# Kernel optimization log

Measured on AMD Instinct MI355X. Metric: run time of the kernel, lower is better.

## Reference

```python
import jax, jax.numpy as jnp
import numpy as np

B, N = 2, 4096
SA, DG, ED, OUT = 128, 1024, 4, 128
RF = 0.1   # ED_radius_factor
EPS = 1e-5  # BatchNorm eps


def setup_inputs() -> dict:
    key = jax.random.key(0)
    ks = jax.random.split(key, 16)
    def w(k, sh, sc=0.05):
        return jax.random.normal(k, sh, jnp.float32) * sc
    return dict(
        pointcloud=jax.random.normal(ks[0], (B, N, 3), jnp.float32),
        h1=jax.random.normal(ks[1], (B, SA, N), jnp.float32),
        h2=jax.random.normal(ks[2], (B, DG, N), jnp.float32),
        dg_w1=w(ks[3], (256, DG)), dg_b1=jnp.zeros(256), dg_g1=jnp.ones(256), dg_be1=jnp.zeros(256),
        dg_w2=w(ks[4], (64, 256)), dg_b2=jnp.zeros(64), dg_g2=jnp.ones(64), dg_be2=jnp.zeros(64),
        dg_w3=w(ks[5], (32, 64)), dg_b3=jnp.zeros(32), dg_g3=jnp.ones(32), dg_be3=jnp.zeros(32),
        ed_w1=w(ks[6], (3, ED), 0.5), ed_b1=jnp.zeros(ED),
        ed_w2=w(ks[7], (ED, ED), 0.5), ed_b2=jnp.zeros(ED),
        w1=w(ks[8], (512, SA + 32 + ED)), b1=jnp.zeros(512), g1=jnp.ones(512), be1=jnp.zeros(512),
        w2=w(ks[9], (256, 512)), b2=jnp.zeros(256), g2=jnp.ones(256), be2=jnp.zeros(256),
        w3=w(ks[10], (OUT, 256)), b3=jnp.zeros(OUT), g3=jnp.ones(OUT), be3=jnp.zeros(OUT),
    )


def _conv1x1(x, w, b):  # x: (B,C,N) 1x1 Conv1d
    return jnp.einsum('oc,bcn->bon', w, x) + b[None, :, None]


def _bn(x, g, b):  # training-mode BatchNorm1d over (B,N) per channel
    m = x.mean(axis=(0, 2), keepdims=True)
    v = ((x - m) ** 2).mean(axis=(0, 2), keepdims=True)
    return g[None, :, None] * (x - m) * jax.lax.rsqrt(v + EPS) + b[None, :, None]


def _eigs(xyz):  # (N,3) -> (N,3) eigenvalues of per-point radius-neighbor covariance
    n = xyz.shape[0]
    x2 = (xyz * xyz).sum(-1)
    d2 = jnp.maximum(x2[:, None] + x2[None, :] - 2.0 * (xyz @ xyz.T), 0.0)
    dist = jnp.sqrt(jnp.maximum(d2, 1e-12))
    eye = jnp.eye(n, dtype=bool)
    max_d = jnp.where(eye, -jnp.inf, dist).max()  # calculate_distances max
    radius = max_d * RF                            # adaptive radius
    mask = ((dist < radius) & ~eye).astype(xyz.dtype)  # (N,N) radius neighbors, no self
    cnt = mask.sum(1)                              # true neighbor count (for the mean)
    mu = (mask @ xyz) / jnp.maximum(cnt, 1.0)[:, None]
    # sum_j m_ij x_j x_j^T via one matmul on flattened outer products
    S = (mask @ (xyz[:, :, None] * xyz[:, None, :]).reshape(n, 9)).reshape(n, 3, 3)
    # NOTE: original divides by k = mask.shape[0] == N (not neighbor count) -- kept faithfully
    cov = (S - cnt[:, None, None] * mu[:, :, None] * mu[:, None, :]) / n
    return jnp.linalg.eigvalsh(cov)


def reference(pointcloud, h1, h2,
              dg_w1, dg_b1, dg_g1, dg_be1,
              dg_w2, dg_b2, dg_g2, dg_be2,
              dg_w3, dg_b3, dg_g3, dg_be3,
              ed_w1, ed_b1, ed_w2, ed_b2,
              w1, b1, g1, be1, w2, b2, g2, be2, w3, b3, g3, be3):
    xyz = pointcloud[..., 0:3]
    # DG head: 1024 -> 256 -> 64 -> 32 (1x1 conv + BN + ReLU)
    f2 = jax.nn.relu(_bn(_conv1x1(h2, dg_w1, dg_b1), dg_g1, dg_be1))
    f2 = jax.nn.relu(_bn(_conv1x1(f2, dg_w2, dg_b2), dg_g2, dg_be2))
    f2 = jax.nn.relu(_bn(_conv1x1(f2, dg_w3, dg_b3), dg_g3, dg_be3))
    # ED branch: per-point local PCA eigenvalues + tiny MLP (3->4->4)
    eig = jax.vmap(_eigs)(xyz)                        # (B,N,3)
    h3 = jax.nn.relu(eig @ ed_w1 + ed_b1) @ ed_w2 + ed_b2  # (B,N,4)
    z = jnp.concatenate([h1, f2, jnp.transpose(h3, (0, 2, 1))], axis=1)  # (B,164,N)
    z = jax.nn.relu(_bn(_conv1x1(z, w1, b1), g1, be1))
    z = jax.nn.relu(_bn(_conv1x1(z, w2, b2), g2, be2))
    z = jax.nn.relu(_bn(_conv1x1(z, w3, b3), g3, be3))
    return (xyz, z)
```

## Files before the change

### kernel.cpp

```cpp
#include <hip/hip_runtime.h>
#include <math.h>

#define NPTS 4096
#define NB 2

typedef __attribute__((ext_vector_type(8))) short short8;
typedef __attribute__((ext_vector_type(4))) float f32x4;
typedef unsigned int uint32;

__device__ __forceinline__ unsigned short f2bf(float f) {
  uint32 u = __float_as_uint(f);
  uint32 r = (u + 0x7FFFu + ((u >> 16) & 1u)) >> 16;
  return (unsigned short)r;
}
__device__ __forceinline__ uint2 pack4(float a, float b, float c, float d) {
  uint2 r;
  r.x = (uint32)f2bf(a) | ((uint32)f2bf(b) << 16);
  r.y = (uint32)f2bf(c) | ((uint32)f2bf(d) << 16);
  return r;
}
__device__ __forceinline__ float bflo(uint32 w) { return __uint_as_float((w & 0xffffu) << 16); }
__device__ __forceinline__ float bfhi(uint32 w) { return __uint_as_float(w & 0xffff0000u); }

struct WArgs {
  const float* src[6];
  unsigned short* dst[6];
};

__device__ __forceinline__ void transpose_tile(const float* __restrict__ src, int C,
                                               unsigned short* __restrict__ dst,
                                               int dstStride, int dstOff, int b, int c0,
                                               int n0) {
  __shared__ float tile[32][33];
  const float* s = src + (size_t)b * C * NPTS;
  int r = threadIdx.x >> 3, q = threadIdx.x & 7;
  float4 v = *(const float4*)(s + (size_t)(c0 + r) * NPTS + n0 + q * 4);
  tile[r][q * 4 + 0] = v.x;
  tile[r][q * 4 + 1] = v.y;
  tile[r][q * 4 + 2] = v.z;
  tile[r][q * 4 + 3] = v.w;
  __syncthreads();
  uint2 o = pack4(tile[q * 4 + 0][r], tile[q * 4 + 1][r], tile[q * 4 + 2][r],
                  tile[q * 4 + 3][r]);
  *(uint2*)(dst + ((size_t)b * NPTS + n0 + r) * dstStride + dstOff + c0 + q * 4) = o;
}

__global__ __launch_bounds__(256)
void prep_all(const float* __restrict__ h2, const float* __restrict__ h1, WArgs wa,
              unsigned short* __restrict__ h2t, unsigned short* __restrict__ Zt,
              unsigned int* __restrict__ mx) {
  int bid = blockIdx.x;
  if (bid < 8192) {
    int b = bid >> 12, r = bid & 4095, ct = r & 31, nt = r >> 5;
    transpose_tile(h2, 1024, h2t, 1024, 0, b, ct * 32, nt * 32);
  } else if (bid < 9216) {
    int r = bid - 8192, b = r >> 9, r2 = r & 511, ct = r2 & 3, nt = r2 >> 2;
    transpose_tile(h1, 128, Zt, 192, 0, b, ct * 32, nt * 32);
  } else if (bid < 9248) {
    int r = bid - 9216;
    for (int idx = r * 256 + threadIdx.x; idx < NB * NPTS * 7; idx += 32 * 256) {
      int u = idx % 7, n = (idx / 7) & (NPTS - 1), b = idx / (7 * NPTS);
      *(uint2*)(Zt + ((size_t)b * NPTS + n) * 192 + 164 + u * 4) = make_uint2(0u, 0u);
    }
  } else if (bid < 9504) {
    const int segKp[6] = {1024, 256, 64, 192, 512, 256};
    const int segM[6] = {256, 64, 32, 512, 256, 128};
    const int segK[6] = {1024, 256, 64, 164, 512, 256};
    const int segEnd[6] = {262144, 278528, 282624, 380928, 512000, 544768};
    int r = bid - 9248;
    for (int idx = r * 256 + threadIdx.x; idx < 544768; idx += 256 * 256) {
      int w = 0, start = 0;
#pragma unroll
      for (int s = 0; s < 6; ++s)
        if (idx >= segEnd[s]) { w = s + 1; start = segEnd[s]; }
      int local = idx - start, Kp = segKp[w], m = local / Kp, k = local % Kp;
      float v = (m < segM[w] && k < segK[w]) ? wa.src[w][m * segK[w] + k] : 0.f;
      wa.dst[w][local] = f2bf(v);
    }
  } else {
    if (threadIdx.x < 2) mx[threadIdx.x] = 0u;
  }
}

template <int BN_IN>
__global__ __launch_bounds__(256)
void gemm_mfma_t(const unsigned short* __restrict__ Wp, const unsigned short* __restrict__ X,
                 const float* __restrict__ aG, const float* __restrict__ bG,
                 unsigned short* __restrict__ Y, float* __restrict__ psum,
                 float* __restrict__ psq, int M, int Mp, int Kp) {
  __shared__ char db[2][9216];
  __shared__ float a_sh[512], b_sh[512];
  const int b = blockIdx.z, nt = blockIdx.x, mt = blockIdx.y;
  const int n0 = nt * 64, m0 = mt * 64;
  const int tid = threadIdx.x, lane = tid & 63, wid = tid >> 6;
  const int wm = wid >> 1, wn = wid & 1, g = lane >> 4, c = lane & 15;
  const int ktiles = Kp >> 6;
  const unsigned short* Xb = X + (size_t)b * NPTS * Kp;

  if (BN_IN) {
    for (int ch = tid; ch < Kp; ch += 256) {
      a_sh[ch] = aG[ch];
      b_sh[ch] = bG[ch];
    }
    __syncthreads();
  }

  uint4 st[2];
  auto loadG = [&](int kt) {
    int k0 = kt << 6;
#pragma unroll
    for (int i = 0; i < 2; ++i) {
      int u = tid + i * 256, n = u >> 3, s = u & 7;
      st[i] = *(const uint4*)(Xb + (size_t)(n0 + n) * Kp + k0 + s * 8);
    }
  };
  auto writeS = [&](int buf, int kt) {
    int k0 = kt << 6;
#pragma unroll
    for (int i = 0; i < 2; ++i) {
      int u = tid + i * 256, n = u >> 3, s = u & 7;
      uint4 v = st[i];
      if (BN_IN) {
        int k = k0 + s * 8;
        float4 a0 = *(const float4*)&a_sh[k], a1 = *(const float4*)&a_sh[k + 4];
        float4 b0 = *(const float4*)&b_sh[k], b1 = *(const float4*)&b_sh[k + 4];
        uint2 lo = pack4(fmaxf(bflo(v.x) * a0.x + b0.x, 0.f),
                         fmaxf(bfhi(v.x) * a0.y + b0.y, 0.f),
                         fmaxf(bflo(v.y) * a0.z + b0.z, 0.f),
                         fmaxf(bfhi(v.y) * a0.w + b0.w, 0.f));
        uint2 hi = pack4(fmaxf(bflo(v.z) * a1.x + b1.x, 0.f),
                         fmaxf(bfhi(v.z) * a1.y + b1.y, 0.f),
                         fmaxf(bflo(v.w) * a1.z + b1.z, 0.f),
                         fmaxf(bfhi(v.w) * a1.w + b1.w, 0.f));
        v = make_uint4(lo.x, lo.y, hi.x, hi.y);
      }
      *(uint4*)&db[buf][u / 8 * 144 + (u & 7) * 16] = v;
      (void)n;
    }
  };
  auto loadA = [&](int kt, uint4* Af) {
    const unsigned short* base = Wp + (size_t)(m0 + wm * 32 + c) * Kp + (kt << 6) + g * 8;
#pragma unroll
    for (int mf = 0; mf < 2; ++mf)
#pragma unroll
      for (int kw = 0; kw < 2; ++kw)
        Af[mf * 2 + kw] = *(const uint4*)(base + (size_t)mf * 16 * Kp + kw * 32);
  };

  f32x4 acc[2][2] = {};
  uint4 Acur[4], Anext[4] = {};
  loadG(0);
  loadA(0, Acur);
  writeS(0, 0);
  __syncthreads();
  int cur = 0;
  for (int t = 0; t < ktiles; ++t) {
    if (t + 1 < ktiles) {
      loadG(t + 1);
      loadA(t + 1, Anext);
    }
#pragma unroll
    for (int kw = 0; kw < 2; ++kw) {
      union { uint4 u; short8 s; } a0, a1;
      a0.u = Acur[0 * 2 + kw];
      a1.u = Acur[1 * 2 + kw];
#pragma unroll
      for (int nf = 0; nf < 2; ++nf) {
        union { uint4 u; short8 s; } bf;
        bf.u = *(const uint4*)&db[cur][(wn * 32 + nf * 16 + c) * 144 + kw * 64 + g * 16];
        acc[0][nf] = __builtin_amdgcn_mfma_f32_16x16x32_bf16(a0.s, bf.s, acc[0][nf], 0, 0, 0);
        acc[1][nf] = __builtin_amdgcn_mfma_f32_16x16x32_bf16(a1.s, bf.s, acc[1][nf], 0, 0, 0);
      }
    }
    if (t + 1 < ktiles) writeS(cur ^ 1, t + 1);
    __syncthreads();
    cur ^= 1;
#pragma unroll
    for (int i = 0; i < 4; ++i) Acur[i] = Anext[i];
  }

#pragma unroll
  for (int nf = 0; nf < 2; ++nf) {
    int n = n0 + wn * 32 + nf * 16 + c;
    unsigned short* yrow = Y + ((size_t)b * NPTS + n) * Mp;
#pragma unroll
    for (int mf = 0; mf < 2; ++mf) {
      int mb = m0 + wm * 32 + mf * 16 + g * 4;
      *(uint2*)(yrow + mb) =
          pack4(acc[mf][nf][0], acc[mf][nf][1], acc[mf][nf][2], acc[mf][nf][3]);
    }
  }
  int slot = b * 128 + nt * 2 + wn;
#pragma unroll
  for (int mf = 0; mf < 2; ++mf)
#pragma unroll
    for (int r = 0; r < 4; ++r) {
      float s = acc[mf][0][r] + acc[mf][1][r];
      float q = acc[mf][0][r] * acc[mf][0][r] + acc[mf][1][r] * acc[mf][1][r];
#pragma unroll
      for (int m = 1; m < 16; m <<= 1) {
        s += __shfl_xor(s, m, 64);
        q += __shfl_xor(q, m, 64);
      }
      int row = m0 + wm * 32 + mf * 16 + g * 4 + r;
      if (c == 0 && row < M) {
        psum[(size_t)row * 256 + slot] = s;
        psq[(size_t)row * 256 + slot] = q;
      }
    }
}

__global__ __launch_bounds__(256)
void bn_finalize(const float* __restrict__ psum, const float* __restrict__ psq,
                 const float* __restrict__ gamma, const float* __restrict__ beta,
                 float* __restrict__ a_, float* __restrict__ b_) {
  int ch = blockIdx.x, t = threadIdx.x;
  float s = psum[(size_t)ch * 256 + t];
  float q = psq[(size_t)ch * 256 + t];
#pragma unroll
  for (int m = 1; m < 64; m <<= 1) {
    s += __shfl_xor(s, m, 64);
    q += __shfl_xor(q, m, 64);
  }
  __shared__ float ws[4][2];
  if ((t & 63) == 0) { ws[t >> 6][0] = s; ws[t >> 6][1] = q; }
  __syncthreads();
  if (t == 0) {
    float S = ws[0][0] + ws[1][0] + ws[2][0] + ws[3][0];
    float Q = ws[0][1] + ws[1][1] + ws[2][1] + ws[3][1];
    const float inv = 1.f / (float)(NB * NPTS);
    float mean = S * inv;
    float var = fmaxf(Q * inv - mean * mean, 0.f);
    float aa = rsqrtf(var + 1e-5f) * gamma[ch];
    a_[ch] = aa;
    b_[ch] = beta[ch] - mean * aa;
  }
}

__global__ __launch_bounds__(256)
void f2_apply(const unsigned short* __restrict__ Y, const float* __restrict__ a_,
              const float* __restrict__ b_, unsigned short* __restrict__ Zt) {
  int idx = blockIdx.x * 256 + threadIdx.x;
  int c4 = idx & 7;
  int n = (idx >> 3) & (NPTS - 1);
  int b = idx >> 15;
  uint2 v = *(const uint2*)(Y + ((size_t)b * NPTS + n) * 64 + c4 * 4);
  float4 aa = ((const float4*)a_)[c4];
  float4 bb = ((const float4*)b_)[c4];
  uint2 o = pack4(fmaxf(bflo(v.x) * aa.x + bb.x, 0.f), fmaxf(bfhi(v.x) * aa.y + bb.y, 0.f),
                  fmaxf(bflo(v.y) * aa.z + bb.z, 0.f), fmaxf(bfhi(v.y) * aa.w + bb.w, 0.f));
  *(uint2*)(Zt + ((size_t)b * NPTS + n) * 192 + 128 + c4 * 4) = o;
}

__global__ __launch_bounds__(256)
void out_final(const unsigned short* __restrict__ Y, const float* __restrict__ a_,
               const float* __restrict__ b_, const float* __restrict__ pc,
               float* __restrict__ out) {
  int bid = blockIdx.x;
  if (bid < 1024) {
    __shared__ float tile[32][33];
    int b = bid >> 9, r0 = bid & 511;
    int c0 = (r0 & 3) * 32, n0 = (r0 >> 2) * 32;
    int r = threadIdx.x >> 3, q = threadIdx.x & 7;
    uint2 v = *(const uint2*)(Y + ((size_t)b * NPTS + n0 + r) * 128 + c0 + q * 4);
    float4 aa = *(const float4*)(a_ + c0 + q * 4);
    float4 bb = *(const float4*)(b_ + c0 + q * 4);
    tile[r][q * 4 + 0] = fmaxf(bflo(v.x) * aa.x + bb.x, 0.f);
    tile[r][q * 4 + 1] = fmaxf(bfhi(v.x) * aa.y + bb.y, 0.f);
    tile[r][q * 4 + 2] = fmaxf(bflo(v.y) * aa.z + bb.z, 0.f);
    tile[r][q * 4 + 3] = fmaxf(bfhi(v.y) * aa.w + bb.w, 0.f);
    __syncthreads();
    float4 o = make_float4(tile[q * 4 + 0][r], tile[q * 4 + 1][r], tile[q * 4 + 2][r],
                           tile[q * 4 + 3][r]);
    float* z = out + (size_t)NB * NPTS * 3;
    *(float4*)(z + ((size_t)b * 128 + c0 + r) * NPTS + n0 + q * 4) = o;
  } else {
    int i = (bid - 1024) * 256 + threadIdx.x;
    ((float4*)out)[i] = ((const float4*)pc)[i];
  }
}

__global__ __launch_bounds__(256)
void maxd2_kernel(const float* __restrict__ pc, unsigned int* __restrict__ mx) {
  __shared__ float4 sp[512];
  __shared__ float lm[4];
  int b = blockIdx.z;
  int j0 = blockIdx.y * 512;
  int i0 = blockIdx.x * 64;
  const float* pb = pc + (size_t)b * NPTS * 3;
  for (int t = threadIdx.x; t < 512; t += 256) {
    int j = j0 + t;
    sp[t] = make_float4(pb[j * 3], pb[j * 3 + 1], pb[j * 3 + 2], 0.f);
  }
  __syncthreads();
  int il = threadIdx.x & 63, sl = threadIdx.x >> 6;
  int i = i0 + il;
  float xi = pb[i * 3], yi = pb[i * 3 + 1], zi = pb[i * 3 + 2];
  float x2i = xi * xi + yi * yi + zi * zi;
  float m = 0.f;
#pragma unroll 4
  for (int j = sl * 128, e = sl * 128 + 128; j < e; ++j) {
    float4 pj = sp[j];
    float x2j = pj.x * pj.x + pj.y * pj.y + pj.z * pj.z;
    float dot = xi * pj.x + yi * pj.y + zi * pj.z;
    m = fmaxf(m, fmaxf(x2i + x2j - 2.f * dot, 0.f));
  }
#pragma unroll
  for (int off = 32; off > 0; off >>= 1) m = fmaxf(m, __shfl_xor(m, off, 64));
  if ((threadIdx.x & 63) == 0) lm[threadIdx.x >> 6] = m;
  __syncthreads();
  if (threadIdx.x == 0) {
    float v = fmaxf(fmaxf(lm[0], lm[1]), fmaxf(lm[2], lm[3]));
    atomicMax(&mx[b], __float_as_uint(v));
  }
}

__global__ __launch_bounds__(256)
void eigs_partial(const float* __restrict__ pc, const unsigned int* __restrict__ mx,
                  float* __restrict__ part) {
  __shared__ float4 sp[1024];
  __shared__ float red[4][32][10];
  int b = blockIdx.z;
  int js = blockIdx.y;
  int j0 = js * 1024;
  int i0 = blockIdx.x * 32;
  const float* pb = pc + (size_t)b * NPTS * 3;
  for (int t = threadIdx.x; t < 1024; t += 256) {
    int j = j0 + t;
    sp[t] = make_float4(pb[j * 3], pb[j * 3 + 1], pb[j * 3 + 2], 0.f);
  }
  __syncthreads();
  int il = threadIdx.x & 31, sl = threadIdx.x >> 5;
  int i = i0 + il;
  float xi = pb[i * 3], yi = pb[i * 3 + 1], zi = pb[i * 3 + 2];
  float x2i = xi * xi + yi * yi + zi * zi;
  float r2 = 0.01f * fmaxf(__uint_as_float(mx[b]), 1e-12f);
  float vals[10];
#pragma unroll
  for (int v = 0; v < 10; ++v) vals[v] = 0.f;
  int iloc = i - j0;
#pragma unroll 2
  for (int j = sl * 128, e = sl * 128 + 128; j < e; ++j) {
    float4 pj = sp[j];
    float x2j = pj.x * pj.x + pj.y * pj.y + pj.z * pj.z;
    float dot = xi * pj.x + yi * pj.y + zi * pj.z;
    float d2 = fmaxf(fmaxf(x2i + x2j - 2.f * dot, 0.f), 1e-12f);
    float msk = ((d2 < r2) && (j != iloc)) ? 1.f : 0.f;
    vals[0] += msk;
    vals[1] = fmaf(msk, pj.x, vals[1]);
    vals[2] = fmaf(msk, pj.y, vals[2]);
    vals[3] = fmaf(msk, pj.z, vals[3]);
    vals[4] = fmaf(msk, pj.x * pj.x, vals[4]);
    vals[5] = fmaf(msk, pj.x * pj.y, vals[5]);
    vals[6] = fmaf(msk, pj.x * pj.z, vals[6]);
    vals[7] = fmaf(msk, pj.y * pj.y, vals[7]);
    vals[8] = fmaf(msk, pj.y * pj.z, vals[8]);
    vals[9] = fmaf(msk, pj.z * pj.z, vals[9]);
  }
#pragma unroll
  for (int v = 0; v < 10; ++v) vals[v] += __shfl_xor(vals[v], 32, 64);
  int w = threadIdx.x >> 6;
  if ((threadIdx.x & 63) < 32)
#pragma unroll
    for (int v = 0; v < 10; ++v) red[w][il][v] = vals[v];
  __syncthreads();
  if (threadIdx.x < 32) {
    int ii = i0 + threadIdx.x;
    size_t base = ((size_t)(b * 4 + js) * 10) * NPTS + ii;
#pragma unroll
    for (int v = 0; v < 10; ++v)
      part[base + (size_t)v * NPTS] = red[0][threadIdx.x][v] + red[1][threadIdx.x][v] +
                                      red[2][threadIdx.x][v] + red[3][threadIdx.x][v];
  }
}

__global__ __launch_bounds__(256)
void eigs_finalize(const float* __restrict__ part, const float* __restrict__ ew1,
                   const float* __restrict__ eb1, const float* __restrict__ ew2,
                   const float* __restrict__ eb2, unsigned short* __restrict__ Zt) {
  int p = blockIdx.x * 256 + threadIdx.x;
  int b = p >> 12, i = p & (NPTS - 1);
  float t[10];
#pragma unroll
  for (int v = 0; v < 10; ++v) {
    float s = 0.f;
#pragma unroll
    for (int js = 0; js < 4; ++js) s += part[((size_t)(b * 4 + js) * 10 + v) * NPTS + i];
    t[v] = s;
  }
  double cntd = (double)t[0];
  double denom = cntd > 1.0 ? cntd : 1.0;
  double mux = t[1] / denom, muy = t[2] / denom, muz = t[3] / denom;
  const double inv_n = 1.0 / (double)NPTS;
  double a00 = ((double)t[4] - cntd * mux * mux) * inv_n;
  double a01 = ((double)t[5] - cntd * mux * muy) * inv_n;
// ... 22 lines not shown
    e0 = q + 2.0 * pp * cos(phi + 2.0943951023931953);
    e1 = 3.0 * q - e0 - e2;
  }
  float eg[3] = {(float)e0, (float)e1, (float)e2};
  float tmp[4];
#pragma unroll
  for (int e = 0; e < 4; ++e) {
    float v = eb1[e];
#pragma unroll
    for (int k = 0; k < 3; ++k) v = fmaf(eg[k], ew1[k * 4 + e], v);
    tmp[e] = fmaxf(v, 0.f);
  }
  float h3[4];
#pragma unroll
  for (int f = 0; f < 4; ++f) {
    float v = eb2[f];
#pragma unroll
    for (int e = 0; e < 4; ++e) v = fmaf(tmp[e], ew2[e * 4 + f], v);
    h3[f] = v;
  }
  *(uint2*)(Zt + ((size_t)b * NPTS + i) * 192 + 160) = pack4(h3[0], h3[1], h3[2], h3[3]);
}

extern "C" void kernel_launch(void* const* d_in, const int* in_sizes, int n_in,
                              void* d_out, int out_size, void* d_ws, size_t ws_size,
                              hipStream_t stream) {
  (void)in_sizes; (void)n_in; (void)out_size; (void)ws_size;
  const float* pc    = (const float*)d_in[0];
  const float* h1    = (const float*)d_in[1];
  const float* h2    = (const float*)d_in[2];
  const float* dgw1  = (const float*)d_in[3];
  const float* dgg1  = (const float*)d_in[5];
  const float* dgbe1 = (const float*)d_in[6];
  const float* dgw2  = (const float*)d_in[7];
  const float* dgg2  = (const float*)d_in[9];
  const float* dgbe2 = (const float*)d_in[10];
  const float* dgw3  = (const float*)d_in[11];
  const float* dgg3  = (const float*)d_in[13];
  const float* dgbe3 = (const float*)d_in[14];
  const float* ew1   = (const float*)d_in[15];
  const float* eb1   = (const float*)d_in[16];
  const float* ew2   = (const float*)d_in[17];
  const float* eb2   = (const float*)d_in[18];
  const float* w1    = (const float*)d_in[19];
  const float* g1    = (const float*)d_in[21];
  const float* be1   = (const float*)d_in[22];
  const float* w2    = (const float*)d_in[23];
  const float* g2    = (const float*)d_in[25];
  const float* be2   = (const float*)d_in[26];
  const float* w3    = (const float*)d_in[27];
  const float* g3    = (const float*)d_in[29];
  const float* be3   = (const float*)d_in[30];
  float* out = (float*)d_out;

  char* p = (char*)d_ws;
  auto take = [&](size_t bytes) { char* r = p; p += (bytes + 255) & ~(size_t)255; return r; };
  unsigned short* h2t = (unsigned short*)take((size_t)NB * NPTS * 1024 * 2);
  unsigned short* Zt  = (unsigned short*)take((size_t)NB * NPTS * 192 * 2);
  unsigned short* wp1 = (unsigned short*)take((size_t)256 * 1024 * 2);
  unsigned short* wp2 = (unsigned short*)take((size_t)64 * 256 * 2);
  unsigned short* wp3 = (unsigned short*)take((size_t)64 * 64 * 2);
  unsigned short* wp4 = (unsigned short*)take((size_t)512 * 192 * 2);
  unsigned short* wp5 = (unsigned short*)take((size_t)256 * 512 * 2);
  unsigned short* wp6 = (unsigned short*)take((size_t)128 * 256 * 2);
  unsigned short* yA  = (unsigned short*)take((size_t)NB * NPTS * 256 * 2);
  unsigned short* yB  = (unsigned short*)take((size_t)NB * NPTS * 512 * 2);
  float* psum = (float*)take((size_t)512 * 256 * 4);
  float* psq  = (float*)take((size_t)512 * 256 * 4);
  float* a_   = (float*)take((size_t)512 * 4);
  float* b_   = (float*)take((size_t)512 * 4);
  float* part = (float*)take((size_t)NB * 4 * 10 * NPTS * 4);
  unsigned int* mx = (unsigned int*)take(256);

  WArgs wa;
  wa.src[0] = dgw1; wa.dst[0] = wp1;
  wa.src[1] = dgw2; wa.dst[1] = wp2;
  wa.src[2] = dgw3; wa.dst[2] = wp3;
  wa.src[3] = w1;   wa.dst[3] = wp4;
  wa.src[4] = w2;   wa.dst[4] = wp5;
  wa.src[5] = w3;   wa.dst[5] = wp6;

  prep_all<<<9505, 256, 0, stream>>>(h2, h1, wa, h2t, Zt, mx);
  maxd2_kernel<<<dim3(NPTS / 64, 8, NB), 256, 0, stream>>>(pc, mx);
  eigs_partial<<<dim3(NPTS / 32, 4, NB), 256, 0, stream>>>(pc, mx, part);
  eigs_finalize<<<NB * NPTS / 256, 256, 0, stream>>>(part, ew1, eb1, ew2, eb2, Zt);

  auto layerD = [&](const unsigned short* Wp, const unsigned short* X, unsigned short* Y,
                    int M, int Mp, int Kp, const float* g, const float* be) {
    gemm_mfma_t<0><<<dim3(64, Mp / 64, NB), 256, 0, stream>>>(Wp, X, a_, b_, Y, psum, psq,
                                                              M, Mp, Kp);
    bn_finalize<<<M, 256, 0, stream>>>(psum, psq, g, be, a_, b_);
  };
  auto layerF = [&](const unsigned short* Wp, const unsigned short* X, unsigned short* Y,
                    int M, int Mp, int Kp, const float* g, const float* be) {
    gemm_mfma_t<1><<<dim3(64, Mp / 64, NB), 256, 0, stream>>>(Wp, X, a_, b_, Y, psum, psq,
                                                              M, Mp, Kp);
    bn_finalize<<<M, 256, 0, stream>>>(psum, psq, g, be, a_, b_);
  };

  layerD(wp1, h2t, yA, 256, 256, 1024, dgg1, dgbe1);
  layerF(wp2, yA, yB, 64, 64, 256, dgg2, dgbe2);
  layerF(wp3, yB, yA, 32, 64, 64, dgg3, dgbe3);
  f2_apply<<<NB * NPTS * 8 / 256, 256, 0, stream>>>(yA, a_, b_, Zt);
  layerD(wp4, Zt, yB, 512, 512, 192, g1, be1);
  layerF(wp5, yB, yA, 256, 256, 512, g2, be2);
  layerF(wp6, yA, yB, 128, 128, 256, g3, be3);
  out_final<<<1048, 256, 0, stream>>>(yB, a_, b_, pc, out);
}
```

Before: 168.4 us.

## Fuse BN finalize into GEMMs, merge maxd2 into prep and eigs into first GEMM

Folds the separate BN-finalize kernels into each GEMM through a last-block atomic counter. The pairwise max-distance pass moves into the prep kernel and the eigen-partial pass runs as extra blocks of the first GEMM. The f2_apply kernel is removed by having layer 3 write into Zt directly, with a per-channel floor vector standing in for ReLU. Transposes use larger 64x64 tiles, and the GEMM double-buffers global loads two tiles ahead. The aim is fewer launches and less serialization, at the cost of more complex ordering through atomics and fences and heavier per-block shared memory.

```diff
diff --git a/kernel.cpp b/kernel.cpp
--- a/kernel.cpp
+++ b/kernel.cpp
@@ -3,6 +3,7 @@
 
 #define NPTS 4096
 #define NB 2
+#define BIGNEG -3.0e38f
 
 typedef __attribute__((ext_vector_type(8))) short short8;
 typedef __attribute__((ext_vector_type(4))) float f32x4;
@@ -22,143 +23,264 @@
 __device__ __forceinline__ float bflo(uint32 w) { return __uint_as_float((w & 0xffffu) << 16); }
 __device__ __forceinline__ float bfhi(uint32 w) { return __uint_as_float(w & 0xffff0000u); }
 
-struct WArgs {
-  const float* src[6];
-  unsigned short* dst[6];
+struct PrepP {
+  const float *h2, *h1, *pc;
+  const float* wsrc[6];
+  unsigned short* wdst[6];
+  unsigned short *h2t, *Zt;
+  float *aZ, *bZ, *fZ, *f0;
+  unsigned int* mx;
 };
 
-__device__ __forceinline__ void transpose_tile(const float* __restrict__ src, int C,
-                                               unsigned short* __restrict__ dst,
-                                               int dstStride, int dstOff, int b, int c0,
-                                               int n0) {
-  __shared__ float tile[32][33];
-  const float* s = src + (size_t)b * C * NPTS;
-  int r = threadIdx.x >> 3, q = threadIdx.x & 7;
-  float4 v = *(const float4*)(s + (size_t)(c0 + r) * NPTS + n0 + q * 4);
-  tile[r][q * 4 + 0] = v.x;
-  tile[r][q * 4 + 1] = v.y;
-  tile[r][q * 4 + 2] = v.z;
-  tile[r][q * 4 + 3] = v.w;
-  __syncthreads();
-  uint2 o = pack4(tile[q * 4 + 0][r], tile[q * 4 + 1][r], tile[q * 4 + 2][r],
-                  tile[q * 4 + 3][r]);
-  *(uint2*)(dst + ((size_t)b * NPTS + n0 + r) * dstStride + dstOff + c0 + q * 4) = o;
-}
+union ShPrep {
+  float tile[64][65];
+  struct { float4 sp[512]; float lm[8]; } m;
+};
 
 __global__ __launch_bounds__(256)
-void prep_all(const float* __restrict__ h2, const float* __restrict__ h1, WArgs wa,
-              unsigned short* __restrict__ h2t, unsigned short* __restrict__ Zt,
-              unsigned int* __restrict__ mx) {
-  int bid = blockIdx.x;
-  if (bid < 8192) {
-    int b = bid >> 12, r = bid & 4095, ct = r & 31, nt = r >> 5;
-    transpose_tile(h2, 1024, h2t, 1024, 0, b, ct * 32, nt * 32);
-  } else if (bid < 9216) {
-    int r = bid - 8192, b = r >> 9, r2 = r & 511, ct = r2 & 3, nt = r2 >> 2;
-    transpose_tile(h1, 128, Zt, 192, 0, b, ct * 32, nt * 32);
-  } else if (bid < 9248) {
-    int r = bid - 9216;
-    for (int idx = r * 256 + threadIdx.x; idx < NB * NPTS * 7; idx += 32 * 256) {
+void prep_maxd2(PrepP P) {
+  __shared__ ShPrep sh;
+  int bid = blockIdx.x, tid = threadIdx.x;
+  if (bid < 2304) {
+    const float* src; unsigned short* dst; int S, C, b, c0, n0;
+    if (bid < 2048) {
+      b = bid >> 10; int r = bid & 1023;
+      c0 = (r & 15) * 64; n0 = (r >> 4) * 64;
+      src = P.h2; dst = P.h2t; S = 1024; C = 1024;
+    } else {
+      int r = bid - 2048; b = r >> 7; int r2 = r & 127;
+      c0 = (r2 & 1) * 64; n0 = (r2 >> 1) * 64;
+      src = P.h1; dst = P.Zt; S = 192; C = 128;
+    }
+    const float* sb = src + (size_t)b * C * NPTS;
+#pragma unroll
+    for (int p = 0; p < 4; ++p) {
+      int r = (tid >> 4) + p * 16, q = tid & 15;
+      float4 v = *(const float4*)(sb + (size_t)(c0 + r) * NPTS + n0 + q * 4);
+      sh.tile[r][q * 4 + 0] = v.x;
+      sh.tile[r][q * 4 + 1] = v.y;
+      sh.tile[r][q * 4 + 2] = v.z;
+      sh.tile[r][q * 4 + 3] = v.w;
+    }
+    __syncthreads();
+#pragma unroll
+    for (int p = 0; p < 2; ++p) {
+      int n = (tid >> 3) + p * 32, j = tid & 7;
+      uint2 lo = pack4(sh.tile[j * 8 + 0][n], sh.tile[j * 8 + 1][n], sh.tile[j * 8 + 2][n],
+                       sh.tile[j * 8 + 3][n]);
+      uint2 hi = pack4(sh.tile[j * 8 + 4][n], sh.tile[j * 8 + 5][n], sh.tile[j * 8 + 6][n],
+                       sh.tile[j * 8 + 7][n]);
+      *(uint4*)(dst + ((size_t)b * NPTS + n0 + n) * S + c0 + j * 8) =
+          make_uint4(lo.x, lo.y, hi.x, hi.y);
+    }
+  } else if (bid < 2336) {
+    int r = bid - 2304;
+    for (int idx = r * 256 + tid; idx < NB * NPTS * 7; idx += 32 * 256) {
       int u = idx % 7, n = (idx / 7) & (NPTS - 1), b = idx / (7 * NPTS);
-      *(uint2*)(Zt + ((size_t)b * NPTS + n) * 192 + 164 + u * 4) = make_uint2(0u, 0u);
-    }
-  } else if (bid < 9504) {
+      *(uint2*)(P.Zt + ((size_t)b * NPTS + n) * 192 + 164 + u * 4) = make_uint2(0u, 0u);
+    }
+  } else if (bid < 2592) {
     const int segKp[6] = {1024, 256, 64, 192, 512, 256};
     const int segM[6] = {256, 64, 32, 512, 256, 128};
     const int segK[6] = {1024, 256, 64, 164, 512, 256};
     const int segEnd[6] = {262144, 278528, 282624, 380928, 512000, 544768};
-    int r = bid - 9248;
-    for (int idx = r * 256 + threadIdx.x; idx < 544768; idx += 256 * 256) {
+    int r = bid - 2336;
+    for (int idx = r * 256 + tid; idx < 544768; idx += 256 * 256) {
       int w = 0, start = 0;
 #pragma unroll
       for (int s = 0; s < 6; ++s)
         if (idx >= segEnd[s]) { w = s + 1; start = segEnd[s]; }
       int local = idx - start, Kp = segKp[w], m = local / Kp, k = local % Kp;
-      float v = (m < segM[w] && k < segK[w]) ? wa.src[w][m * segK[w] + k] : 0.f;
-      wa.dst[w][local] = f2bf(v);
+      float v = (m < segM[w] && k < segK[w]) ? P.wsrc[w][m * segK[w] + k] : 0.f;
+      P.wdst[w][local] = f2bf(v);
+    }
+  } else if (bid == 2592) {
+    for (int ch = tid; ch < 512; ch += 256) {
+      P.f0[ch] = 0.f;
+      if (ch < 192) { P.aZ[ch] = 1.f; P.bZ[ch] = 0.f; P.fZ[ch] = BIGNEG; }
     }
   } else {
-    if (threadIdx.x < 2) mx[threadIdx.x] = 0u;
-  }
-}
-
-template <int BN_IN>
+    int vb = bid - 2593;
+    int b = vb >> 9, rem = vb & 511, it = rem & 63, jt = rem >> 6;
+    int i0 = it * 64, j0 = jt * 512;
+    const float* pb = P.pc + (size_t)b * NPTS * 3;
+    for (int t = tid; t < 512; t += 256) {
+      int j = j0 + t;
+      float x = pb[j * 3], y = pb[j * 3 + 1], z = pb[j * 3 + 2];
+      sh.m.sp[t] = make_float4(x, y, z, fmaf(x, x, fmaf(y, y, z * z)));
+    }
+    __syncthreads();
+    int il = tid & 63, sl = tid >> 6;
+    int i = i0 + il;
+    float xi = pb[i * 3], yi = pb[i * 3 + 1], zi = pb[i * 3 + 2];
+    float x2i = fmaf(xi, xi, fmaf(yi, yi, zi * zi));
+    float m = 0.f;
+#pragma unroll 4
+    for (int j = sl * 128, e2 = sl * 128 + 128; j < e2; ++j) {
+      float4 pj = sh.m.sp[j];
+      float dot = fmaf(xi, pj.x, fmaf(yi, pj.y, zi * pj.z));
+      m = fmaxf(m, fmaf(-2.f, dot, x2i + pj.w));
+    }
+#pragma unroll
+    for (int off = 32; off > 0; off >>= 1) m = fmaxf(m, __shfl_xor(m, off, 64));
+    if ((tid & 63) == 0) sh.m.lm[tid >> 6] = m;
+    __syncthreads();
+    if (tid == 0) {
+      float v = fmaxf(fmaxf(sh.m.lm[0], sh.m.lm[1]), fmaxf(sh.m.lm[2], sh.m.lm[3]));
+      atomicMax(&P.mx[b], __float_as_uint(v));
+    }
+  }
+}
+
+struct GemmP {
+  const unsigned short* Wp;
+  const unsigned short* X;
+  const float *aIn, *bIn, *fIn;
+  unsigned short* Y;
+  int Ystride;
+  const float *gam, *bet;
+  float *aOut, *bOut, *fOut;
+  unsigned int* cnt;
+  float *psum, *psq;
+  int M, Kp, ngb;
+};
+
+union ShGemm {
+  struct { char db[2][9216]; float ash[512], bsh[512], fsh[512]; } g;
+  struct { float4 sp[1024]; float red[4][32][10]; } e;
+};
+
+template <int BN_IN, int WITH_EIG>
 __global__ __launch_bounds__(256)
-void gemm_mfma_t(const unsigned short* __restrict__ Wp, const unsigned short* __restrict__ X,
-                 const float* __restrict__ aG, const float* __restrict__ bG,
-                 unsigned short* __restrict__ Y, float* __restrict__ psum,
-                 float* __restrict__ psq, int M, int Mp, int Kp) {
-  __shared__ char db[2][9216];
-  __shared__ float a_sh[512], b_sh[512];
+void gemm_k(GemmP P, const float* __restrict__ pc, const unsigned int* __restrict__ mx,
+            float* __restrict__ part) {
+  __shared__ ShGemm sh;
+  __shared__ unsigned int lastf;
+  const int tid = threadIdx.x;
+
+  if (WITH_EIG && blockIdx.z >= NB) {
+    int e = blockIdx.x + 64 * blockIdx.y + 256 * (blockIdx.z - NB);
+    int b = e >> 9, rem = e & 511, it = rem & 127, js = rem >> 7;
+    int i0 = it * 32, j0 = js * 1024;
+    const float* pb = pc + (size_t)b * NPTS * 3;
+    for (int t = tid; t < 1024; t += 256) {
+      int j = j0 + t;
+      float x = pb[j * 3], y = pb[j * 3 + 1], z = pb[j * 3 + 2];
+      sh.e.sp[t] = make_float4(x, y, z, fmaf(x, x, fmaf(y, y, z * z)));
+    }
+    __syncthreads();
+    int il = tid & 31, sl = tid >> 5;
+    int i = i0 + il;
+    float xi = pb[i * 3], yi = pb[i * 3 + 1], zi = pb[i * 3 + 2];
+    float x2i = fmaf(xi, xi, fmaf(yi, yi, zi * zi));
+    float r2 = 0.01f * fmaxf(__uint_as_float(mx[b]), 1e-12f);
+    float v0 = 0, v1 = 0, v2 = 0, v3 = 0, v4 = 0, v5 = 0, v6 = 0, v7 = 0, v8 = 0, v9 = 0;
+#pragma unroll 2
+    for (int j = sl * 128, e2 = sl * 128 + 128; j < e2; ++j) {
+      float4 pj = sh.e.sp[j];
+      float dot = fmaf(xi, pj.x, fmaf(yi, pj.y, zi * pj.z));
+      float d2 = fmaf(-2.f, dot, x2i + pj.w);
+      float msk = d2 < r2 ? 1.f : 0.f;
+      float qx = msk * pj.x, qy = msk * pj.y, qz = msk * pj.z;
+      v0 += msk; v1 += qx; v2 += qy; v3 += qz;
+      v4 = fmaf(qx, pj.x, v4); v5 = fmaf(qx, pj.y, v5); v6 = fmaf(qx, pj.z, v6);
+      v7 = fmaf(qy, pj.y, v7); v8 = fmaf(qy, pj.z, v8); v9 = fmaf(qz, pj.z, v9);
+    }
+    int iloc = i - j0;
+    if (iloc >= sl * 128 && iloc < sl * 128 + 128) {
+      v0 -= 1.f; v1 -= xi; v2 -= yi; v3 -= zi;
+      v4 = fmaf(-xi, xi, v4); v5 = fmaf(-xi, yi, v5); v6 = fmaf(-xi, zi, v6);
+      v7 = fmaf(-yi, yi, v7); v8 = fmaf(-yi, zi, v8); v9 = fmaf(-zi, zi, v9);
+    }
+    float vals[10] = {v0, v1, v2, v3, v4, v5, v6, v7, v8, v9};
+#pragma unroll
+    for (int v = 0; v < 10; ++v) vals[v] += __shfl_xor(vals[v], 32, 64);
+    int w = tid >> 6;
+    if ((tid & 63) < 32)
+#pragma unroll
+      for (int v = 0; v < 10; ++v) sh.e.red[w][il][v] = vals[v];
+    __syncthreads();
+    if (tid < 32) {
+      int ii = i0 + tid;
+      size_t base = ((size_t)(b * 4 + js) * 10) * NPTS + ii;
+#pragma unroll
+      for (int v = 0; v < 10; ++v)
+        part[base + (size_t)v * NPTS] =
+            sh.e.red[0][tid][v] + sh.e.red[1][tid][v] + sh.e.red[2][tid][v] + sh.e.red[3][tid][v];
+    }
+    return;
+  }
+
   const int b = blockIdx.z, nt = blockIdx.x, mt = blockIdx.y;
   const int n0 = nt * 64, m0 = mt * 64;
-  const int tid = threadIdx.x, lane = tid & 63, wid = tid >> 6;
+  const int lane = tid & 63, wid = tid >> 6;
   const int wm = wid >> 1, wn = wid & 1, g = lane >> 4, c = lane & 15;
-  const int ktiles = Kp >> 6;
-  const unsigned short* Xb = X + (size_t)b * NPTS * Kp;
+  const int kt = P.Kp >> 6;
+  const unsigned short* Xb = P.X + (size_t)b * NPTS * P.Kp;
 
   if (BN_IN) {
-    for (int ch = tid; ch < Kp; ch += 256) {
-      a_sh[ch] = aG[ch];
-      b_sh[ch] = bG[ch];
-    }
-    __syncthreads();
-  }
-
-  uint4 st[2];
-  auto loadG = [&](int kt) {
-    int k0 = kt << 6;
+    for (int ch = tid; ch < P.Kp; ch += 256) {
+      sh.g.ash[ch] = P.aIn[ch];
+      sh.g.bsh[ch] = P.bIn[ch];
+      sh.g.fsh[ch] = P.fIn[ch];
+    }
+    __syncthreads();
+  }
+
+  uint4 R0[2], R1[2];
+  auto loadG = [&](int t, uint4* R) {
+    int k0 = t << 6;
 #pragma unroll
     for (int i = 0; i < 2; ++i) {
       int u = tid + i * 256, n = u >> 3, s = u & 7;
-      st[i] = *(const uint4*)(Xb + (size_t)(n0 + n) * Kp + k0 + s * 8);
+      R[i] = *(const uint4*)(Xb + (size_t)(n0 + n) * P.Kp + k0 + s * 8);
     }
   };
-  auto writeS = [&](int buf, int kt) {
-    int k0 = kt << 6;
+  auto writeS = [&](int buf, int t, uint4* R) {
+    int k0 = t << 6;
 #pragma unroll
     for (int i = 0; i < 2; ++i) {
-      int u = tid + i * 256, n = u >> 3, s = u & 7;
-      uint4 v = st[i];
+      int u = tid + i * 256, s = u & 7;
+      uint4 v = R[i];
       if (BN_IN) {
         int k = k0 + s * 8;
-        float4 a0 = *(const float4*)&a_sh[k], a1 = *(const float4*)&a_sh[k + 4];
-        float4 b0 = *(const float4*)&b_sh[k], b1 = *(const float4*)&b_sh[k + 4];
-        uint2 lo = pack4(fmaxf(bflo(v.x) * a0.x + b0.x, 0.f),
-                         fmaxf(bfhi(v.x) * a0.y + b0.y, 0.f),
-                         fmaxf(bflo(v.y) * a0.z + b0.z, 0.f),
-                         fmaxf(bfhi(v.y) * a0.w + b0.w, 0.f));
-        uint2 hi = pack4(fmaxf(bflo(v.z) * a1.x + b1.x, 0.f),
-                         fmaxf(bfhi(v.z) * a1.y + b1.y, 0.f),
-                         fmaxf(bflo(v.w) * a1.z + b1.z, 0.f),
-                         fmaxf(bfhi(v.w) * a1.w + b1.w, 0.f));
+        float4 a0 = *(const float4*)&sh.g.ash[k], a1 = *(const float4*)&sh.g.ash[k + 4];
+        float4 b0 = *(const float4*)&sh.g.bsh[k], b1 = *(const float4*)&sh.g.bsh[k + 4];
+        float4 f0 = *(const float4*)&sh.g.fsh[k], f1 = *(const float4*)&sh.g.fsh[k + 4];
+        uint2 lo = pack4(fmaxf(fmaf(bflo(v.x), a0.x, b0.x), f0.x),
+                         fmaxf(fmaf(bfhi(v.x), a0.y, b0.y), f0.y),
+                         fmaxf(fmaf(bflo(v.y), a0.z, b0.z), f0.z),
+                         fmaxf(fmaf(bfhi(v.y), a0.w, b0.w), f0.w));
+        uint2 hi = pack4(fmaxf(fmaf(bflo(v.z), a1.x, b1.x), f1.x),
+                         fmaxf(fmaf(bfhi(v.z), a1.y, b1.y), f1.y),
+                         fmaxf(fmaf(bflo(v.w), a1.z, b1.z), f1.z),
+                         fmaxf(fmaf(bfhi(v.w), a1.w, b1.w), f1.w));
         v = make_uint4(lo.x, lo.y, hi.x, hi.y);
       }
-      *(uint4*)&db[buf][u / 8 * 144 + (u & 7) * 16] = v;
-      (void)n;
+      *(uint4*)&sh.g.db[buf][(u >> 3) * 144 + (u & 7) * 16] = v;
     }
   };
-  auto loadA = [&](int kt, uint4* Af) {
-    const unsigned short* base = Wp + (size_t)(m0 + wm * 32 + c) * Kp + (kt << 6) + g * 8;
+  auto loadA = [&](int t, uint4* Af) {
+    const unsigned short* base = P.Wp + (size_t)(m0 + wm * 32 + c) * P.Kp + (t << 6) + g * 8;
 #pragma unroll
     for (int mf = 0; mf < 2; ++mf)
 #pragma unroll
       for (int kw = 0; kw < 2; ++kw)
-        Af[mf * 2 + kw] = *(const uint4*)(base + (size_t)mf * 16 * Kp + kw * 32);
+        Af[mf * 2 + kw] = *(const uint4*)(base + (size_t)mf * 16 * P.Kp + kw * 32);
   };
 
   f32x4 acc[2][2] = {};
   uint4 Acur[4], Anext[4] = {};
-  loadG(0);
+  loadG(0, R0);
   loadA(0, Acur);
-  writeS(0, 0);
+  writeS(0, 0, R0);
+  if (kt > 1) loadG(1, R1);
   __syncthreads();
   int cur = 0;
-  for (int t = 0; t < ktiles; ++t) {
-    if (t + 1 < ktiles) {
-      loadG(t + 1);
-      loadA(t + 1, Anext);
-    }
+
+  auto step = [&](int t, uint4* Rload, uint4* Rwrite) {
+    if (t + 2 < kt) loadG(t + 2, Rload);
+    if (t + 1 < kt) loadA(t + 1, Anext);
 #pragma unroll
     for (int kw = 0; kw < 2; ++kw) {
       union { uint4 u; short8 s; } a0, a1;
@@ -167,27 +289,35 @@
 #pragma unroll
       for (int nf = 0; nf < 2; ++nf) {
         union { uint4 u; short8 s; } bf;
-        bf.u = *(const uint4*)&db[cur][(wn * 32 + nf * 16 + c) * 144 + kw * 64 + g * 16];
+        bf.u = *(const uint4*)&sh.g.db[cur][(wn * 32 + nf * 16 + c) * 144 + kw * 64 + g * 16];
         acc[0][nf] = __builtin_amdgcn_mfma_f32_16x16x32_bf16(a0.s, bf.s, acc[0][nf], 0, 0, 0);
         acc[1][nf] = __builtin_amdgcn_mfma_f32_16x16x32_bf16(a1.s, bf.s, acc[1][nf], 0, 0, 0);
       }
     }
-    if (t + 1 < ktiles) writeS(cur ^ 1, t + 1);
+    if (t + 1 < kt) writeS(cur ^ 1, t + 1, Rwrite);
     __syncthreads();
     cur ^= 1;
 #pragma unroll
     for (int i = 0; i < 4; ++i) Acur[i] = Anext[i];
+  };
+  for (int t = 0; t < kt;) {
+    step(t, R0, R1);
+    ++t;
+    if (t >= kt) break;
+    step(t, R1, R0);
+    ++t;
   }
 
 #pragma unroll
   for (int nf = 0; nf < 2; ++nf) {
     int n = n0 + wn * 32 + nf * 16 + c;
-    unsigned short* yrow = Y + ((size_t)b * NPTS + n) * Mp;
+    unsigned short* yrow = P.Y + ((size_t)b * NPTS + n) * P.Ystride;
 #pragma unroll
     for (int mf = 0; mf < 2; ++mf) {
       int mb = m0 + wm * 32 + mf * 16 + g * 4;
-      *(uint2*)(yrow + mb) =
-          pack4(acc[mf][nf][0], acc[mf][nf][1], acc[mf][nf][2], acc[mf][nf][3]);
+      if (mb < P.M)
+        *(uint2*)(yrow + mb) =
+            pack4(acc[mf][nf][0], acc[mf][nf][1], acc[mf][nf][2], acc[mf][nf][3]);
     }
   }
   int slot = b * 128 + nt * 2 + wn;
@@ -203,174 +333,35 @@
         q += __shfl_xor(q, m, 64);
       }
       int row = m0 + wm * 32 + mf * 16 + g * 4 + r;
-      if (c == 0 && row < M) {
-        psum[(size_t)row * 256 + slot] = s;
-        psq[(size_t)row * 256 + slot] = q;
+      if (c == 0 && row < P.M) {
+        P.psum[(size_t)row * 256 + slot] = s;
+        P.psq[(size_t)row * 256 + slot] = q;
       }
     }
-}
-
-__global__ __launch_bounds__(256)
-void bn_finalize(const float* __restrict__ psum, const float* __restrict__ psq,
-                 const float* __restrict__ gamma, const float* __restrict__ beta,
-                 float* __restrict__ a_, float* __restrict__ b_) {
-  int ch = blockIdx.x, t = threadIdx.x;
-  float s = psum[(size_t)ch * 256 + t];
-  float q = psq[(size_t)ch * 256 + t];
-#pragma unroll
-  for (int m = 1; m < 64; m <<= 1) {
-    s += __shfl_xor(s, m, 64);
-    q += __shfl_xor(q, m, 64);
-  }
-  __shared__ float ws[4][2];
-  if ((t & 63) == 0) { ws[t >> 6][0] = s; ws[t >> 6][1] = q; }
+
+  __threadfence();
+  if (tid == 0) lastf = (atomicAdd(P.cnt, 1u) == (unsigned)(P.ngb - 1)) ? 1u : 0u;
   __syncthreads();
-  if (t == 0) {
-    float S = ws[0][0] + ws[1][0] + ws[2][0] + ws[3][0];
-    float Q = ws[0][1] + ws[1][1] + ws[2][1] + ws[3][1];
-    const float inv = 1.f / (float)(NB * NPTS);
-    float mean = S * inv;
-    float var = fmaxf(Q * inv - mean * mean, 0.f);
-    float aa = rsqrtf(var + 1e-5f) * gamma[ch];
-    a_[ch] = aa;
-    b_[ch] = beta[ch] - mean * aa;
-  }
-}
-
-__global__ __launch_bounds__(256)
-void f2_apply(const unsigned short* __restrict__ Y, const float* __restrict__ a_,
-              const float* __restrict__ b_, unsigned short* __restrict__ Zt) {
-  int idx = blockIdx.x * 256 + threadIdx.x;
-  int c4 = idx & 7;
-  int n = (idx >> 3) & (NPTS - 1);
-  int b = idx >> 15;
-  uint2 v = *(const uint2*)(Y + ((size_t)b * NPTS + n) * 64 + c4 * 4);
-  float4 aa = ((const float4*)a_)[c4];
-  float4 bb = ((const float4*)b_)[c4];
-  uint2 o = pack4(fmaxf(bflo(v.x) * aa.x + bb.x, 0.f), fmaxf(bfhi(v.x) * aa.y + bb.y, 0.f),
-                  fmaxf(bflo(v.y) * aa.z + bb.z, 0.f), fmaxf(bfhi(v.y) * aa.w + bb.w, 0.f));
-  *(uint2*)(Zt + ((size_t)b * NPTS + n) * 192 + 128 + c4 * 4) = o;
-}
-
-__global__ __launch_bounds__(256)
-void out_final(const unsigned short* __restrict__ Y, const float* __restrict__ a_,
-               const float* __restrict__ b_, const float* __restrict__ pc,
-               float* __restrict__ out) {
-  int bid = blockIdx.x;
-  if (bid < 1024) {
-    __shared__ float tile[32][33];
-    int b = bid >> 9, r0 = bid & 511;
-    int c0 = (r0 & 3) * 32, n0 = (r0 >> 2) * 32;
-    int r = threadIdx.x >> 3, q = threadIdx.x & 7;
-    uint2 v = *(const uint2*)(Y + ((size_t)b * NPTS + n0 + r) * 128 + c0 + q * 4);
-    float4 aa = *(const float4*)(a_ + c0 + q * 4);
-    float4 bb = *(const float4*)(b_ + c0 + q * 4);
-    tile[r][q * 4 + 0] = fmaxf(bflo(v.x) * aa.x + bb.x, 0.f);
-    tile[r][q * 4 + 1] = fmaxf(bfhi(v.x) * aa.y + bb.y, 0.f);
-    tile[r][q * 4 + 2] = fmaxf(bflo(v.y) * aa.z + bb.z, 0.f);
-    tile[r][q * 4 + 3] = fmaxf(bfhi(v.y) * aa.w + bb.w, 0.f);
-    __syncthreads();
-    float4 o = make_float4(tile[q * 4 + 0][r], tile[q * 4 + 1][r], tile[q * 4 + 2][r],
-                           tile[q * 4 + 3][r]);
-    float* z = out + (size_t)NB * NPTS * 3;
-    *(float4*)(z + ((size_t)b * 128 + c0 + r) * NPTS + n0 + q * 4) = o;
-  } else {
-    int i = (bid - 1024) * 256 + threadIdx.x;
-    ((float4*)out)[i] = ((const float4*)pc)[i];
-  }
-}
-
-__global__ __launch_bounds__(256)
-void maxd2_kernel(const float* __restrict__ pc, unsigned int* __restrict__ mx) {
-  __shared__ float4 sp[512];
-  __shared__ float lm[4];
-  int b = blockIdx.z;
-  int j0 = blockIdx.y * 512;
-  int i0 = blockIdx.x * 64;
-  const float* pb = pc + (size_t)b * NPTS * 3;
-  for (int t = threadIdx.x; t < 512; t += 256) {
-    int j = j0 + t;
-    sp[t] = make_float4(pb[j * 3], pb[j * 3 + 1], pb[j * 3 + 2], 0.f);
-  }
-  __syncthreads();
-  int il = threadIdx.x & 63, sl = threadIdx.x >> 6;
-  int i = i0 + il;
-  float xi = pb[i * 3], yi = pb[i * 3 + 1], zi = pb[i * 3 + 2];
-  float x2i = xi * xi + yi * yi + zi * zi;
-  float m = 0.f;
+  if (lastf) {
+    for (int ch = tid; ch < P.M; ch += 256) {
+      const float4* s4 = (const float4*)(P.psum + (size_t)ch * 256);
+      const float4* q4 = (const float4*)(P.psq + (size_t)ch * 256);
+      float s = 0.f, q = 0.f;
 #pragma unroll 4
-  for (int j = sl * 128, e = sl * 128 + 128; j < e; ++j) {
-    float4 pj = sp[j];
-    float x2j = pj.x * pj.x + pj.y * pj.y + pj.z * pj.z;
-    float dot = xi * pj.x + yi * pj.y + zi * pj.z;
-    m = fmaxf(m, fmaxf(x2i + x2j - 2.f * dot, 0.f));
-  }
-#pragma unroll
-  for (int off = 32; off > 0; off >>= 1) m = fmaxf(m, __shfl_xor(m, off, 64));
-  if ((threadIdx.x & 63) == 0) lm[threadIdx.x >> 6] = m;
-  __syncthreads();
-  if (threadIdx.x == 0) {
-    float v = fmaxf(fmaxf(lm[0], lm[1]), fmaxf(lm[2], lm[3]));
-    atomicMax(&mx[b], __float_as_uint(v));
-  }
-}
-
-__global__ __launch_bounds__(256)
-void eigs_partial(const float* __restrict__ pc, const unsigned int* __restrict__ mx,
-                  float* __restrict__ part) {
-  __shared__ float4 sp[1024];
-  __shared__ float red[4][32][10];
-  int b = blockIdx.z;
-  int js = blockIdx.y;
-  int j0 = js * 1024;
-  int i0 = blockIdx.x * 32;
-  const float* pb = pc + (size_t)b * NPTS * 3;
-  for (int t = threadIdx.x; t < 1024; t += 256) {
-    int j = j0 + t;
-    sp[t] = make_float4(pb[j * 3], pb[j * 3 + 1], pb[j * 3 + 2], 0.f);
-  }
-  __syncthreads();
-  int il = threadIdx.x & 31, sl = threadIdx.x >> 5;
-  int i = i0 + il;
-  float xi = pb[i * 3], yi = pb[i * 3 + 1], zi = pb[i * 3 + 2];
-  float x2i = xi * xi + yi * yi + zi * zi;
-  float r2 = 0.01f * fmaxf(__uint_as_float(mx[b]), 1e-12f);
-  float vals[10];
-#pragma unroll
-  for (int v = 0; v < 10; ++v) vals[v] = 0.f;
-  int iloc = i - j0;
-#pragma unroll 2
-  for (int j = sl * 128, e = sl * 128 + 128; j < e; ++j) {
-    float4 pj = sp[j];
-    float x2j = pj.x * pj.x + pj.y * pj.y + pj.z * pj.z;
-    float dot = xi * pj.x + yi * pj.y + zi * pj.z;
-    float d2 = fmaxf(fmaxf(x2i + x2j - 2.f * dot, 0.f), 1e-12f);
-    float msk = ((d2 < r2) && (j != iloc)) ? 1.f : 0.f;
-    vals[0] += msk;
-    vals[1] = fmaf(msk, pj.x, vals[1]);
-    vals[2] = fmaf(msk, pj.y, vals[2]);
-    vals[3] = fmaf(msk, pj.z, vals[3]);
-    vals[4] = fmaf(msk, pj.x * pj.x, vals[4]);
-    vals[5] = fmaf(msk, pj.x * pj.y, vals[5]);
-    vals[6] = fmaf(msk, pj.x * pj.z, vals[6]);
-    vals[7] = fmaf(msk, pj.y * pj.y, vals[7]);
-    vals[8] = fmaf(msk, pj.y * pj.z, vals[8]);
-    vals[9] = fmaf(msk, pj.z * pj.z, vals[9]);
-  }
-#pragma unroll
-  for (int v = 0; v < 10; ++v) vals[v] += __shfl_xor(vals[v], 32, 64);
-  int w = threadIdx.x >> 6;
-  if ((threadIdx.x & 63) < 32)
-#pragma unroll
-    for (int v = 0; v < 10; ++v) red[w][il][v] = vals[v];
-  __syncthreads();
-  if (threadIdx.x < 32) {
-    int ii = i0 + threadIdx.x;
-    size_t base = ((size_t)(b * 4 + js) * 10) * NPTS + ii;
-#pragma unroll
-    for (int v = 0; v < 10; ++v)
-      part[base + (size_t)v * NPTS] = red[0][threadIdx.x][v] + red[1][threadIdx.x][v] +
-                                      red[2][threadIdx.x][v] + red[3][threadIdx.x][v];
+      for (int i = 0; i < 64; ++i) {
+        float4 a = s4[i];
+        s += a.x + a.y + a.z + a.w;
+        float4 w = q4[i];
+        q += w.x + w.y + w.z + w.w;
+      }
+      const float inv = 1.f / 8192.f;
+      float mean = s * inv;
+      float var = fmaxf(q * inv - mean * mean, 0.f);
+      float aa = rsqrtf(var + 1e-5f) * P.gam[ch];
+      P.aOut[ch] = aa;
+      P.bOut[ch] = P.bet[ch] - mean * aa;
+      if (P.fOut) P.fOut[ch] = 0.f;
+    }
   }
 }
 
@@ -439,6 +430,34 @@
   *(uint2*)(Zt + ((size_t)b * NPTS + i) * 192 + 160) = pack4(h3[0], h3[1], h3[2], h3[3]);
 }
 
+__global__ __launch_bounds__(256)
+void out_final(const unsigned short* __restrict__ Y, const float* __restrict__ a_,
+               const float* __restrict__ b_, const float* __restrict__ pc,
+               float* __restrict__ out) {
+  int bid = blockIdx.x;
+  if (bid < 1024) {
+    __shared__ float tile[32][33];
+    int b = bid >> 9, r0 = bid & 511;
+    int c0 = (r0 & 3) * 32, n0 = (r0 >> 2) * 32;
+    int r = threadIdx.x >> 3, q = threadIdx.x & 7;
+    uint2 v = *(const uint2*)(Y + ((size_t)b * NPTS + n0 + r) * 128 + c0 + q * 4);
+    float4 aa = *(const float4*)(a_ + c0 + q * 4);
+    float4 bb = *(const float4*)(b_ + c0 + q * 4);
+    tile[r][q * 4 + 0] = fmaxf(bflo(v.x) * aa.x + bb.x, 0.f);
+    tile[r][q * 4 + 1] = fmaxf(bfhi(v.x) * aa.y + bb.y, 0.f);
+    tile[r][q * 4 + 2] = fmaxf(bflo(v.y) * aa.z + bb.z, 0.f);
+    tile[r][q * 4 + 3] = fmaxf(bfhi(v.y) * aa.w + bb.w, 0.f);
+    __syncthreads();
+    float4 o = make_float4(tile[q * 4 + 0][r], tile[q * 4 + 1][r], tile[q * 4 + 2][r],
+                           tile[q * 4 + 3][r]);
+    float* z = out + (size_t)NB * NPTS * 3;
+    *(float4*)(z + ((size_t)b * 128 + c0 + r) * NPTS + n0 + q * 4) = o;
+  } else {
+    int i = (bid - 1024) * 256 + threadIdx.x;
+    ((float4*)out)[i] = ((const float4*)pc)[i];
+  }
+}
+
 extern "C" void kernel_launch(void* const* d_in, const int* in_sizes, int n_in,
                               void* d_out, int out_size, void* d_ws, size_t ws_size,
                               hipStream_t stream) {
@@ -472,6 +491,7 @@
 
   char* p = (char*)d_ws;
   auto take = [&](size_t bytes) { char* r = p; p += (bytes + 255) & ~(size_t)255; return r; };
+  unsigned int* cntmx = (unsigned int*)take(64);
   unsigned short* h2t = (unsigned short*)take((size_t)NB * NPTS * 1024 * 2);
   unsigned short* Zt  = (unsigned short*)take((size_t)NB * NPTS * 192 * 2);
   unsigned short* wp1 = (unsigned short*)take((size_t)256 * 1024 * 2);
@@ -484,43 +504,56 @@
   unsigned short* yB  = (unsigned short*)take((size_t)NB * NPTS * 512 * 2);
   float* psum = (float*)take((size_t)512 * 256 * 4);
   float* psq  = (float*)take((size_t)512 * 256 * 4);
-  float* a_   = (float*)take((size_t)512 * 4);
-  float* b_   = (float*)take((size_t)512 * 4);
+  float* a1 = (float*)take(512 * 4); float* b1 = (float*)take(512 * 4);
+  float* a2 = (float*)take(512 * 4); float* b2 = (float*)take(512 * 4);
+  float* aZ = (float*)take(512 * 4); float* bZ = (float*)take(512 * 4);
+  float* fZ = (float*)take(512 * 4);
+  float* a4 = (float*)take(512 * 4); float* b4 = (float*)take(512 * 4);
+  float* a5 = (float*)take(512 * 4); float* b5 = (float*)take(512 * 4);
+  float* a6 = (float*)take(512 * 4); float* b6 = (float*)take(512 * 4);
+  float* f0 = (float*)take(512 * 4);
   float* part = (float*)take((size_t)NB * 4 * 10 * NPTS * 4);
-  unsigned int* mx = (unsigned int*)take(256);
-
-  WArgs wa;
-  wa.src[0] = dgw1; wa.dst[0] = wp1;
-  wa.src[1] = dgw2; wa.dst[1] = wp2;
-  wa.src[2] = dgw3; wa.dst[2] = wp3;
-  wa.src[3] = w1;   wa.dst[3] = wp4;
-  wa.src[4] = w2;   wa.dst[4] = wp5;
-  wa.src[5] = w3;   wa.dst[5] = wp6;
-
-  prep_all<<<9505, 256, 0, stream>>>(h2, h1, wa, h2t, Zt, mx);
-  maxd2_kernel<<<dim3(NPTS / 64, 8, NB), 256, 0, stream>>>(pc, mx);
-  eigs_partial<<<dim3(NPTS / 32, 4, NB), 256, 0, stream>>>(pc, mx, part);
+  unsigned int* cnt = cntmx;
+  unsigned int* mx = cntmx + 8;
+
+  hipMemsetAsync(cntmx, 0, 64, stream);
+
+  PrepP PP;
+  PP.h2 = h2; PP.h1 = h1; PP.pc = pc;
+  PP.wsrc[0] = dgw1; PP.wsrc[1] = dgw2; PP.wsrc[2] = dgw3;
+  PP.wsrc[3] = w1;   PP.wsrc[4] = w2;   PP.wsrc[5] = w3;
+  PP.wdst[0] = wp1; PP.wdst[1] = wp2; PP.wdst[2] = wp3;
+  PP.wdst[3] = wp4; PP.wdst[4] = wp5; PP.wdst[5] = wp6;
+  PP.h2t = h2t; PP.Zt = Zt;
+  PP.aZ = aZ; PP.bZ = bZ; PP.fZ = fZ; PP.f0 = f0;
+  PP.mx = mx;
+  prep_maxd2<<<3617, 256, 0, stream>>>(PP);
+
+  GemmP L1 = {wp1, h2t, nullptr, nullptr, nullptr, yA, 256, dgg1, dgbe1,
+              a1, b1, nullptr, cnt + 0, psum, psq, 256, 1024, 64 * 4 * NB};
+  gemm_k<0, 1><<<dim3(64, 4, NB + 4), 256, 0, stream>>>(L1, pc, mx, part);
+
   eigs_finalize<<<NB * NPTS / 256, 256, 0, stream>>>(part, ew1, eb1, ew2, eb2, Zt);
 
-  auto layerD = [&](const unsigned short* Wp, const unsigned short* X, unsigned short* Y,
-                    int M, int Mp, int Kp, const float* g, const float* be) {
-    gemm_mfma_t<0><<<dim3(64, Mp / 64, NB), 256, 0, stream>>>(Wp, X, a_, b_, Y, psum, psq,
-                                                              M, Mp, Kp);
-    bn_finalize<<<M, 256, 0, stream>>>(psum, psq, g, be, a_, b_);
-  };
-  auto layerF = [&](const unsigned short* Wp, const unsigned short* X, unsigned short* Y,
-                    int M, int Mp, int Kp, const float* g, const float* be) {
-    gemm_mfma_t<1><<<dim3(64, Mp / 64, NB), 256, 0, stream>>>(Wp, X, a_, b_, Y, psum, psq,
-                                                              M, Mp, Kp);
-    bn_finalize<<<M, 256, 0, stream>>>(psum, psq, g, be, a_, b_);
-  };
-
-  layerD(wp1, h2t, yA, 256, 256, 1024, dgg1, dgbe1);
-  layerF(wp2, yA, yB, 64, 64, 256, dgg2, dgbe2);
-  layerF(wp3, yB, yA, 32, 64, 64, dgg3, dgbe3);
-  f2_apply<<<NB * NPTS * 8 / 256, 256, 0, stream>>>(yA, a_, b_, Zt);
-  layerD(wp4, Zt, yB, 512, 512, 192, g1, be1);
-  layerF(wp5, yB, yA, 256, 256, 512, g2, be2);
-  layerF(wp6, yA, yB, 128, 128, 256, g3, be3);
-  out_final<<<1048, 256, 0, stream>>>(yB, a_, b_, pc, out);
-}
+  GemmP L2 = {wp2, yA, a1, b1, f0, yB, 64, dgg2, dgbe2,
+              a2, b2, nullptr, cnt + 1, psum, psq, 64, 256, 64 * 1 * NB};
+  gemm_k<1, 0><<<dim3(64, 1, NB), 256, 0, stream>>>(L2, pc, mx, part);
+
+  GemmP L3 = {wp3, yB, a2, b2, f0, Zt + 128, 192, dgg3, dgbe3,
+              aZ + 128, bZ + 128, fZ + 128, cnt + 2, psum, psq, 32, 64, 64 * 1 * NB};
+  gemm_k<1, 0><<<dim3(64, 1, NB), 256, 0, stream>>>(L3, pc, mx, part);
+
+  GemmP L4 = {wp4, Zt, aZ, bZ, fZ, yB, 512, g1, be1,
+              a4, b4, nullptr, cnt + 3, psum, psq, 512, 192, 64 * 8 * NB};
+  gemm_k<1, 0><<<dim3(64, 8, NB), 256, 0, stream>>>(L4, pc, mx, part);
+
+  GemmP L5 = {wp5, yB, a4, b4, f0, yA, 256, g2, be2,
+              a5, b5, nullptr, cnt + 4, psum, psq, 256, 512, 64 * 4 * NB};
+  gemm_k<1, 0><<<dim3(64, 4, NB), 256, 0, stream>>>(L5, pc, mx, part);
+
+  GemmP L6 = {wp6, yA, a5, b5, f0, yB, 128, g3, be3,
+              a6, b6, nullptr, cnt + 5, psum, psq, 128, 256, 64 * 2 * NB};
+  gemm_k<1, 0><<<dim3(64, 2, NB), 256, 0, stream>>>(L6, pc, mx, part);
+
+  out_final<<<1048, 256, 0, stream>>>(yB, a6, b6, pc, out);
+}
```

New measurement: 486.4 us. 2.89x slower.
